# Kernel optimization log

Hardware: AMD Instinct MI355X
Metric: run time of the kernel (lower is better)

The kernel has to match this reference:

```python
import jax, jax.numpy as jnp
import numpy as np

LAMBDA_CONT = 0.01
SIGMA = 1.0


def _pairwise_dist(x):
    # Euclidean cdist(x, x): [N, N]
    sq = jnp.sum(x * x, axis=-1)  # [N]
    d2 = sq[:, None] + sq[None, :] - 2.0 * (x @ x.T)
    d2 = jnp.maximum(d2, 0.0)
    # safe sqrt (grad 0 at 0, matching torch.cdist subgradient)
    return jnp.where(d2 > 0, jnp.sqrt(jnp.where(d2 > 0, d2, 1.0)), 0.0)


def setup_inputs() -> dict:
    key = jax.random.key(0)
    k1, k2 = jax.random.split(key)
    points = jax.random.normal(k1, (8192, 2), dtype=jnp.float32)
    outputs = jax.random.uniform(k2, (8192, 8), dtype=jnp.float32)
    return {"points": points, "outputs": outputs}


def reference(points, outputs):
    n = points.shape[0]
    dist = _pairwise_dist(points)                     # [N, N]
    weights = jnp.exp(-(dist * dist) / (2.0 * SIGMA ** 2))
    weights = weights * (1.0 - jnp.eye(n, dtype=points.dtype))
    diff = _pairwise_dist(outputs)                    # [N, N]
    loss = jnp.sum(weights * diff) / (n * (n - 1))
    return LAMBDA_CONT * loss
```

## Files before the change

kernel.cpp:

```cpp
#include <hip/hip_runtime.h>


typedef float v2f __attribute__((ext_vector_type(2)));
typedef float v4f __attribute__((ext_vector_type(4)));
typedef _Float16 h4 __attribute__((ext_vector_type(4)));
typedef float f32x4 __attribute__((ext_vector_type(4)));

constexpr int N_PTS = 8192;
constexpr int TDIM  = N_PTS / 64;
constexpr int NBLOCKS = TDIM * (TDIM + 1) / 2;

constexpr float KE = -0.72134752044448169f;
constexpr float M2 =  1.4426950408889634f;

__device__ __forceinline__ int tri_before(int r) {
    return r * TDIM - (r * (r - 1)) / 2;
}

__global__ __launch_bounds__(64, 6) void cont_pairs(
    const float* __restrict__ points, const float* __restrict__ outputs,
    double* __restrict__ partials)
{
    const int b = blockIdx.x;
    int ti = (int)((2 * TDIM + 1 -
                    sqrtf((float)((2 * TDIM + 1) * (2 * TDIM + 1) - 8 * b))) * 0.5f);
    ti = ti < 0 ? 0 : (ti > TDIM - 1 ? TDIM - 1 : ti);
    while (tri_before(ti + 1) <= b) ++ti;
    while (tri_before(ti) > b) --ti;
    const int tj = ti + (b - tri_before(ti));
    const bool diag = (ti == tj);

    const int lane = threadIdx.x;
    const int q = lane >> 4, cl = lane & 15;
    const int rowbase = ti * 64, colbase = tj * 64;

    const _Float16 h0 = (_Float16)0.f, h1 = (_Float16)1.f;

    h4 aO[4], aP[4];
    #pragma unroll
    for (int it = 0; it < 4; ++it) {
        const int i = rowbase + it * 16 + cl;
        const v4f* o = reinterpret_cast<const v4f*>(outputs + 8 * i);
        const v4f x = o[0], y = o[1];
        const v4f s = x * x + y * y;
        const float on = (s.x + s.y) + (s.z + s.w);
        const v2f p = reinterpret_cast<const v2f*>(points)[i];
        const float pn = p.x * p.x + p.y * p.y;
        h4 a;
        if (q == 0)      a = h4{(_Float16)x.x, (_Float16)x.y, (_Float16)x.z, (_Float16)x.w};
        else if (q == 1) a = h4{(_Float16)y.x, (_Float16)y.y, (_Float16)y.z, (_Float16)y.w};
        else if (q == 2) a = h4{(_Float16)on, h1, h0, h0};
        else             a = h4{h0, h0, h0, h0};
        aO[it] = a;
        if (q == 0) aP[it] = h4{(_Float16)p.x, (_Float16)p.y, (_Float16)(KE * pn), h1};
        else        aP[it] = h4{h0, h0, h0, h0};
    }

    float accS = 0.f;

    #pragma unroll 2
    for (int jt = 0; jt < 4; ++jt) {
        const int j = colbase + jt * 16 + cl;
        const v4f* o = reinterpret_cast<const v4f*>(outputs + 8 * j);
        const v4f x = o[0], y = o[1];
        const v4f s = x * x + y * y;
        const float on = (s.x + s.y) + (s.z + s.w);
        const v2f p = reinterpret_cast<const v2f*>(points)[j];
        const float pn = p.x * p.x + p.y * p.y;
        h4 bO, bP;
        if (q == 0)      bO = h4{(_Float16)(-2.f * x.x), (_Float16)(-2.f * x.y),
                                 (_Float16)(-2.f * x.z), (_Float16)(-2.f * x.w)};
        else if (q == 1) bO = h4{(_Float16)(-2.f * y.x), (_Float16)(-2.f * y.y),
                                 (_Float16)(-2.f * y.z), (_Float16)(-2.f * y.w)};
        else if (q == 2) bO = h4{h1, (_Float16)on, h0, h0};
        else             bO = h4{h0, h0, h0, h0};
        if (q == 0) bP = h4{(_Float16)(M2 * p.x), (_Float16)(M2 * p.y), h1,
                            (_Float16)(KE * pn)};
        else        bP = h4{h0, h0, h0, h0};

        #pragma unroll
        for (int it = 0; it < 4; ++it) {
            const f32x4 z = {0.f, 0.f, 0.f, 0.f};
            f32x4 dO = __builtin_amdgcn_mfma_f32_16x16x16f16(aO[it], bO, z, 0, 0, 0);
            f32x4 dP = __builtin_amdgcn_mfma_f32_16x16x16f16(aP[it], bP, z, 0, 0, 0);
            #pragma unroll
            for (int e = 0; e < 4; ++e) {
                float diff = __builtin_amdgcn_sqrtf(fmaxf(dO[e], 0.f));
                if (diag) {
                    const int irow = it * 16 + q * 4 + e;
                    const int jcol = jt * 16 + cl;
                    diff = (jcol > irow) ? diff : 0.f;
                }
                accS = fmaf(__builtin_amdgcn_exp2f(dP[e]), diff, accS);
            }
        }
    }

    #pragma unroll
    for (int off = 32; off > 0; off >>= 1)
        accS += __shfl_down(accS, off, 64);
    if (lane == 0) partials[b] = (double)accS;
}

__global__ __launch_bounds__(1024) void cont_final(
    const double* __restrict__ partials, int nparts,
    float* __restrict__ out, double scale)
{
    const int tid = threadIdx.x;
    double sum = 0.0;
    for (int i = tid; i < nparts; i += 1024) sum += partials[i];
    #pragma unroll
    for (int off = 32; off > 0; off >>= 1)
        sum += __shfl_down(sum, off, 64);

    __shared__ double ws[1024 / 64];
    if ((tid & 63) == 0) ws[tid >> 6] = sum;
    __syncthreads();
    if (tid == 0) {
        double t = 0.0;
        #pragma unroll
        for (int w = 0; w < 1024 / 64; ++w) t += ws[w];
        out[0] = (float)(t * scale);
    }
}

extern "C" void kernel_launch(void* const* d_in, const int* in_sizes, int n_in,
                              void* d_out, int out_size, void* d_ws, size_t ws_size,
                              hipStream_t stream) {
    const float* points  = (const float*)d_in[0];
    const float* outputs = (const float*)d_in[1];
    float* out = (float*)d_out;

    const int n = in_sizes[0] / 2;
    double* partials = (double*)d_ws;

    cont_pairs<<<dim3(NBLOCKS), dim3(64), 0, stream>>>(points, outputs, partials);

    const double scale = 0.01 * 2.0 / ((double)n * (double)(n - 1));
    cont_final<<<1, 1024, 0, stream>>>(partials, NBLOCKS, out, scale);
}
```

Measured before the change: 27.67 us.

## Pack four tile-waves per block, prefetch column data, split accumulators

Each 256-thread block now handles four triangular tiles, one per wave, with an in-block shared-memory reduction. The final kernel shrinks to 256 threads. Inside the loop, the next column chunk's outputs and points are prefetched while the current one is processed, and the loop is fully unrolled. The single accumulator is split into four to shorten the FMA dependency chain. The aim is to cut launch and scheduling overhead, hide load latency, and raise ILP, at the cost of more registers and a block-level barrier. NTILES = 8256 divides evenly by 4.

```diff
diff --git a/kernel.cpp b/kernel.cpp
--- a/kernel.cpp
+++ b/kernel.cpp
@@ -6,9 +6,11 @@
 typedef _Float16 h4 __attribute__((ext_vector_type(4)));
 typedef float f32x4 __attribute__((ext_vector_type(4)));
 
-constexpr int N_PTS = 8192;
-constexpr int TDIM  = N_PTS / 64;
-constexpr int NBLOCKS = TDIM * (TDIM + 1) / 2;
+constexpr int N_PTS  = 8192;
+constexpr int TDIM   = N_PTS / 64;
+constexpr int NTILES = TDIM * (TDIM + 1) / 2;
+constexpr int WPB    = 4;
+constexpr int NBLOCKS = NTILES / WPB;
 
 constexpr float KE = -0.72134752044448169f;
 constexpr float M2 =  1.4426950408889634f;
@@ -17,20 +19,23 @@
     return r * TDIM - (r * (r - 1)) / 2;
 }
 
-__global__ __launch_bounds__(64, 6) void cont_pairs(
+__global__ __launch_bounds__(256, 6) void cont_pairs(
     const float* __restrict__ points, const float* __restrict__ outputs,
     double* __restrict__ partials)
 {
-    const int b = blockIdx.x;
+    const int tid  = threadIdx.x;
+    const int wid  = tid >> 6;
+    const int lane = tid & 63;
+    const int g    = blockIdx.x * WPB + wid;
+
     int ti = (int)((2 * TDIM + 1 -
-                    sqrtf((float)((2 * TDIM + 1) * (2 * TDIM + 1) - 8 * b))) * 0.5f);
+                    sqrtf((float)((2 * TDIM + 1) * (2 * TDIM + 1) - 8 * g))) * 0.5f);
     ti = ti < 0 ? 0 : (ti > TDIM - 1 ? TDIM - 1 : ti);
-    while (tri_before(ti + 1) <= b) ++ti;
-    while (tri_before(ti) > b) --ti;
-    const int tj = ti + (b - tri_before(ti));
+    while (tri_before(ti + 1) <= g) ++ti;
+    while (tri_before(ti) > g) --ti;
+    const int tj = ti + (g - tri_before(ti));
     const bool diag = (ti == tj);
 
-    const int lane = threadIdx.x;
     const int q = lane >> 4, cl = lane & 15;
     const int rowbase = ti * 64, colbase = tj * 64;
 
@@ -56,27 +61,39 @@
         else        aP[it] = h4{h0, h0, h0, h0};
     }
 
-    float accS = 0.f;
+    float accE[4] = {0.f, 0.f, 0.f, 0.f};
 
-    #pragma unroll 2
+    v4f jx, jy; v2f jp;
+    {
+        const int j = colbase + cl;
+        const v4f* o = reinterpret_cast<const v4f*>(outputs + 8 * j);
+        jx = o[0]; jy = o[1];
+        jp = reinterpret_cast<const v2f*>(points)[j];
+    }
+
+    #pragma unroll
     for (int jt = 0; jt < 4; ++jt) {
-        const int j = colbase + jt * 16 + cl;
-        const v4f* o = reinterpret_cast<const v4f*>(outputs + 8 * j);
-        const v4f x = o[0], y = o[1];
-        const v4f s = x * x + y * y;
+        const v4f s = jx * jx + jy * jy;
         const float on = (s.x + s.y) + (s.z + s.w);
-        const v2f p = reinterpret_cast<const v2f*>(points)[j];
-        const float pn = p.x * p.x + p.y * p.y;
+        const float pn = jp.x * jp.x + jp.y * jp.y;
         h4 bO, bP;
-        if (q == 0)      bO = h4{(_Float16)(-2.f * x.x), (_Float16)(-2.f * x.y),
-                                 (_Float16)(-2.f * x.z), (_Float16)(-2.f * x.w)};
-        else if (q == 1) bO = h4{(_Float16)(-2.f * y.x), (_Float16)(-2.f * y.y),
-                                 (_Float16)(-2.f * y.z), (_Float16)(-2.f * y.w)};
+        if (q == 0)      bO = h4{(_Float16)(-2.f * jx.x), (_Float16)(-2.f * jx.y),
+                                 (_Float16)(-2.f * jx.z), (_Float16)(-2.f * jx.w)};
+        else if (q == 1) bO = h4{(_Float16)(-2.f * jy.x), (_Float16)(-2.f * jy.y),
+                                 (_Float16)(-2.f * jy.z), (_Float16)(-2.f * jy.w)};
         else if (q == 2) bO = h4{h1, (_Float16)on, h0, h0};
         else             bO = h4{h0, h0, h0, h0};
-        if (q == 0) bP = h4{(_Float16)(M2 * p.x), (_Float16)(M2 * p.y), h1,
+        if (q == 0) bP = h4{(_Float16)(M2 * jp.x), (_Float16)(M2 * jp.y), h1,
                             (_Float16)(KE * pn)};
         else        bP = h4{h0, h0, h0, h0};
+        const int jcol = jt * 16 + cl;
+
+        if (jt < 3) {
+            const int jn = colbase + (jt + 1) * 16 + cl;
+            const v4f* o = reinterpret_cast<const v4f*>(outputs + 8 * jn);
+            jx = o[0]; jy = o[1];
+            jp = reinterpret_cast<const v2f*>(points)[jn];
+        }
 
         #pragma unroll
         for (int it = 0; it < 4; ++it) {
@@ -88,38 +105,47 @@
                 float diff = __builtin_amdgcn_sqrtf(fmaxf(dO[e], 0.f));
                 if (diag) {
                     const int irow = it * 16 + q * 4 + e;
-                    const int jcol = jt * 16 + cl;
                     diff = (jcol > irow) ? diff : 0.f;
                 }
-                accS = fmaf(__builtin_amdgcn_exp2f(dP[e]), diff, accS);
+                accE[e] = fmaf(__builtin_amdgcn_exp2f(dP[e]), diff, accE[e]);
             }
         }
     }
 
+    float accS = (accE[0] + accE[1]) + (accE[2] + accE[3]);
     #pragma unroll
     for (int off = 32; off > 0; off >>= 1)
         accS += __shfl_down(accS, off, 64);
-    if (lane == 0) partials[b] = (double)accS;
+
+    __shared__ float wpart[WPB];
+    if (lane == 0) wpart[wid] = accS;
+    __syncthreads();
+    if (tid == 0) {
+        double d = 0.0;
+        #pragma unroll
+        for (int w = 0; w < WPB; ++w) d += (double)wpart[w];
+        partials[blockIdx.x] = d;
+    }
 }
 
-__global__ __launch_bounds__(1024) void cont_final(
+__global__ __launch_bounds__(256) void cont_final(
     const double* __restrict__ partials, int nparts,
     float* __restrict__ out, double scale)
 {
     const int tid = threadIdx.x;
     double sum = 0.0;
-    for (int i = tid; i < nparts; i += 1024) sum += partials[i];
+    for (int i = tid; i < nparts; i += 256) sum += partials[i];
     #pragma unroll
     for (int off = 32; off > 0; off >>= 1)
         sum += __shfl_down(sum, off, 64);
 
-    __shared__ double ws[1024 / 64];
+    __shared__ double ws[256 / 64];
     if ((tid & 63) == 0) ws[tid >> 6] = sum;
     __syncthreads();
     if (tid == 0) {
         double t = 0.0;
         #pragma unroll
-        for (int w = 0; w < 1024 / 64; ++w) t += ws[w];
+        for (int w = 0; w < 256 / 64; ++w) t += ws[w];
         out[0] = (float)(t * scale);
     }
 }
@@ -134,8 +160,8 @@
     const int n = in_sizes[0] / 2;
     double* partials = (double*)d_ws;
 
-    cont_pairs<<<dim3(NBLOCKS), dim3(64), 0, stream>>>(points, outputs, partials);
+    cont_pairs<<<dim3(NBLOCKS), dim3(256), 0, stream>>>(points, outputs, partials);
 
     const double scale = 0.01 * 2.0 / ((double)n * (double)(n - 1));
-    cont_final<<<1, 1024, 0, stream>>>(partials, NBLOCKS, out, scale);
+    cont_final<<<1, 256, 0, stream>>>(partials, NBLOCKS, out, scale);
 }
```

Result: slower. 64.54 us (+133.3%).
